# Optimization experiments

Hardware: AMD Instinct MI355X
Metric: run time of the kernel (lower is better)

The kernel has to match this reference:

```python
import jax, jax.numpy as jnp
import numpy as np

EMBED_DIM = 4096
LOW_RANK = 512
BATCH = 8192
K_SEL = 128


def setup_inputs() -> dict:
    key = jax.random.key(0)
    k1, k2, k3, k4 = jax.random.split(key, 4)
    base = jax.random.normal(k1, (BATCH, EMBED_DIM), dtype=jnp.float32)
    source = jax.random.normal(k2, (BATCH, EMBED_DIM), dtype=jnp.float32)
    # fast path: only subspaces[0] is used (all examples share the same index set)
    row = jax.random.randint(k3, (1, K_SEL), 0, LOW_RANK)
    subspaces = jnp.broadcast_to(row, (BATCH, K_SEL)).astype(jnp.int64)
    # orthogonal (column-orthonormal) rotation weight, as produced by
    # torch.nn.utils.parametrizations.orthogonal on [embed_dim, low_rank]
    W, _ = jnp.linalg.qr(jax.random.normal(k4, (EMBED_DIM, LOW_RANK), dtype=jnp.float32))
    return {"base": base, "source": source, "subspaces": subspaces, "W": W}


def reference(base, source, subspaces, W):
    # rotated_base / rotated_source: [B, r]
    # diff in rotated space, gather selected subspace columns, project back.
    sel = subspaces[0]                      # [k] shared index set (fast path)
    diff = (source - base) @ W              # [B, r]
    diff_sel = diff[:, sel]                 # [B, k]
    W_sel = W[:, sel]                       # [d, k]
    out = base + diff_sel @ W_sel.T         # [B, d]
    return out.astype(base.dtype)
```

## Files before the change

### kernel.cpp

```cpp
#include <hip/hip_runtime.h>
#include <hip/hip_bf16.h>

typedef __attribute__((ext_vector_type(4))) float  f32x4;
typedef __attribute__((ext_vector_type(8))) short  short8;
typedef __attribute__((ext_vector_type(4))) short  short4v;

#define EMBED 4096
#define LR    512
#define KSEL  128
#define BATCH 8192

__device__ __forceinline__ short f2bf(float x) {
  union { float f; unsigned u; } c; c.f = x;
  unsigned r = c.u + 0x7FFFu + ((c.u >> 16) & 1u);
  return (short)(r >> 16);
}

__global__ __launch_bounds__(256) void pack_w_kernel(
    const float* __restrict__ W, const int* __restrict__ sel,
    short* __restrict__ Wp, short* __restrict__ Wtp) {
  int idx = blockIdx.x * 256 + threadIdx.x;
  int e = idx >> 7;
  int c = idx & 127;
  int r = sel[c];
  short v = f2bf(W[e * LR + r]);
  Wp [(((e >> 3) << 7) + c) * 8 + (e & 7)] = v;
  Wtp[(((c >> 3) << 12) + e) * 8 + (c & 7)] = v;
}

__global__ __launch_bounds__(256) void gemm1_kernel(
    const float* __restrict__ base, const float* __restrict__ src,
    const short* __restrict__ Wp, short* __restrict__ Tp) {
  __shared__ short Dl[1024];
  const int t  = threadIdx.x;
  const int w  = t >> 6, l = t & 63;
  const int lr = l & 15, lg = l >> 4;
  const int row0 = blockIdx.x * 16;

  const int sr = t >> 4, sk = (t & 15) * 4;
  const float* bp = base + (size_t)(row0 + sr) * EMBED + sk;
  const float* sp = src  + (size_t)(row0 + sr) * EMBED + sk;
  const int wofs = (((sk >> 3) << 4) + sr) * 8 + (sk & 7);

  const short* wpb = Wp + ((lg << 7) + (w << 5) + lr) * 8;

  f32x4 acc0 = {0.f, 0.f, 0.f, 0.f}, acc1 = {0.f, 0.f, 0.f, 0.f};

  f32x4 vb = *(const f32x4*)bp;
  f32x4 vs = *(const f32x4*)sp;

  for (int kt = 0; kt < 64; ++kt) {
    __syncthreads();
    short4v d;
    #pragma unroll
    for (int c = 0; c < 4; ++c) d[c] = f2bf(vs[c] - vb[c]);
    *(short4v*)&Dl[wofs] = d;
    if (kt < 63) {
      vb = *(const f32x4*)(bp + (kt + 1) * 64);
      vs = *(const f32x4*)(sp + (kt + 1) * 64);
    }
    __syncthreads();
    const int kc = kt * 64;
    #pragma unroll
    for (int ks = 0; ks < 2; ++ks) {
      short8 a  = *(const short8*)&Dl[((ks * 4 + lg) << 7) + lr * 8];
      short8 b0 = *(const short8*)(wpb + kc * 128 + ks * 4096);
      short8 b1 = *(const short8*)(wpb + kc * 128 + ks * 4096 + 128);
      acc0 = __builtin_amdgcn_mfma_f32_16x16x32_bf16(a, b0, acc0, 0, 0, 0);
      acc1 = __builtin_amdgcn_mfma_f32_16x16x32_bf16(a, b1, acc1, 0, 0, 0);
    }
  }

  #pragma unroll
  for (int nf = 0; nf < 2; ++nf) {
    f32x4 a = nf ? acc1 : acc0;
    int kk = (w << 5) + (nf << 4) + lr;
    short* dst = Tp + (size_t)(((kk >> 3) << 13) + row0 + (lg << 2)) * 8 + (kk & 7);
    #pragma unroll
    for (int r = 0; r < 4; ++r) dst[r * 8] = f2bf(a[r]);
  }
}

__global__ __launch_bounds__(256) void gemm2_kernel(
    const float* __restrict__ base, const short* __restrict__ Tp,
    const short* __restrict__ Wtp, float* __restrict__ out) {
  const int t  = threadIdx.x;
  const int w  = t >> 6, l = t & 63;
  const int lr = l & 15, lg = l >> 4;
  const int mt = blockIdx.x >> 4, nt = blockIdx.x & 15;
  const int row0 = mt * 64;
  const int col0 = nt * 256 + w * 64;

  short8 afr[4][4];
  #pragma unroll
  for (int m = 0; m < 4; ++m)
    #pragma unroll
    for (int ks = 0; ks < 4; ++ks)
      afr[m][ks] = *(const short8*)(Tp + (size_t)(((ks * 4 + lg) << 13) + row0 + m * 16 + lr) * 8);

  f32x4 acc[4][4];
  #pragma unroll
  for (int m = 0; m < 4; ++m)
    #pragma unroll
    for (int nf = 0; nf < 4; ++nf) acc[m][nf] = (f32x4){0.f, 0.f, 0.f, 0.f};

  #pragma unroll
  for (int nf = 0; nf < 4; ++nf) {
    short8 bfr[4];
    #pragma unroll
    for (int ks = 0; ks < 4; ++ks)
      bfr[ks] = *(const short8*)(Wtp + (size_t)(((ks * 4 + lg) << 12) + col0 + nf * 16 + lr) * 8);
    #pragma unroll
    for (int m = 0; m < 4; ++m)
      #pragma unroll
      for (int ks = 0; ks < 4; ++ks)
        acc[m][nf] = __builtin_amdgcn_mfma_f32_16x16x32_bf16(afr[m][ks], bfr[ks], acc[m][nf], 0, 0, 0);
  }

  #pragma unroll
  for (int m = 0; m < 4; ++m)
    #pragma unroll
    for (int r = 0; r < 4; ++r) {
      const size_t row = row0 + m * 16 + lg * 4 + r;
      #pragma unroll
      for (int nf = 0; nf < 4; ++nf) {
        const size_t o = row * EMBED + col0 + nf * 16 + lr;
        out[o] = base[o] + acc[m][nf][r];
      }
    }
}

extern "C" void kernel_launch(void* const* d_in, const int* in_sizes, int n_in,
                              void* d_out, int out_size, void* d_ws, size_t ws_size,
                              hipStream_t stream) {
  const float* base = (const float*)d_in[0];
  const float* src  = (const float*)d_in[1];
  const int*   sub  = (const int*)d_in[2];
  const float* W    = (const float*)d_in[3];
  float* out = (float*)d_out;

  short* Wp  = (short*)d_ws;
  short* Wtp = Wp  + EMBED * KSEL;
  short* Tp  = Wtp + EMBED * KSEL;

  pack_w_kernel<<<EMBED * KSEL / 256, 256, 0, stream>>>(W, sub, Wp, Wtp);
  gemm1_kernel<<<BATCH / 16, 256, 0, stream>>>(base, src, Wp, Tp);
  gemm2_kernel<<<(BATCH / 64) * 16, 256, 0, stream>>>(base, Tp, Wtp, out);
}
```

Baseline: 140.4 us.

## Split gemm1 K dimension across eight waves with LDS reduction, drop per-step syncs

```diff
diff --git a/kernel.cpp b/kernel.cpp
--- a/kernel.cpp
+++ b/kernel.cpp
@@ -3,7 +3,6 @@
 
 typedef __attribute__((ext_vector_type(4))) float  f32x4;
 typedef __attribute__((ext_vector_type(8))) short  short8;
-typedef __attribute__((ext_vector_type(4))) short  short4v;
 
 #define EMBED 4096
 #define LR    512
@@ -28,56 +27,55 @@
   Wtp[(((c >> 3) << 12) + e) * 8 + (c & 7)] = v;
 }
 
-__global__ __launch_bounds__(256) void gemm1_kernel(
+__global__ __launch_bounds__(512) void gemm1_kernel(
     const float* __restrict__ base, const float* __restrict__ src,
     const short* __restrict__ Wp, short* __restrict__ Tp) {
-  __shared__ short Dl[1024];
+  __shared__ f32x4 red[8 * 8 * 64];
   const int t  = threadIdx.x;
   const int w  = t >> 6, l = t & 63;
   const int lr = l & 15, lg = l >> 4;
   const int row0 = blockIdx.x * 16;
+  const int k0 = w * 512;
 
-  const int sr = t >> 4, sk = (t & 15) * 4;
-  const float* bp = base + (size_t)(row0 + sr) * EMBED + sk;
-  const float* sp = src  + (size_t)(row0 + sr) * EMBED + sk;
-  const int wofs = (((sk >> 3) << 4) + sr) * 8 + (sk & 7);
+  const float* bp = base + (size_t)(row0 + lr) * EMBED + k0 + lg * 8;
+  const float* sp = src  + (size_t)(row0 + lr) * EMBED + k0 + lg * 8;
 
-  const short* wpb = Wp + ((lg << 7) + (w << 5) + lr) * 8;
+  f32x4 acc[8];
+  #pragma unroll
+  for (int nf = 0; nf < 8; ++nf) acc[nf] = (f32x4){0.f, 0.f, 0.f, 0.f};
 
-  f32x4 acc0 = {0.f, 0.f, 0.f, 0.f}, acc1 = {0.f, 0.f, 0.f, 0.f};
-
-  f32x4 vb = *(const f32x4*)bp;
-  f32x4 vs = *(const f32x4*)sp;
-
-  for (int kt = 0; kt < 64; ++kt) {
-    __syncthreads();
-    short4v d;
+  #pragma unroll 4
+  for (int it = 0; it < 16; ++it) {
+    const int kb = it * 32;
+    f32x4 b0 = *(const f32x4*)(bp + kb);
+    f32x4 b1 = *(const f32x4*)(bp + kb + 4);
+    f32x4 s0 = *(const f32x4*)(sp + kb);
+    f32x4 s1 = *(const f32x4*)(sp + kb + 4);
+    short8 a;
     #pragma unroll
-    for (int c = 0; c < 4; ++c) d[c] = f2bf(vs[c] - vb[c]);
-    *(short4v*)&Dl[wofs] = d;
-    if (kt < 63) {
-      vb = *(const f32x4*)(bp + (kt + 1) * 64);
-      vs = *(const f32x4*)(sp + (kt + 1) * 64);
+    for (int j = 0; j < 4; ++j) {
+      a[j]     = f2bf(s0[j] - b0[j]);
+      a[4 + j] = f2bf(s1[j] - b1[j]);
     }
-    __syncthreads();
-    const int kc = kt * 64;
+    const int e = k0 + kb + lg * 8;
+    const short8* wrow = (const short8*)Wp + ((e >> 3) << 7);
     #pragma unroll
-    for (int ks = 0; ks < 2; ++ks) {
-      short8 a  = *(const short8*)&Dl[((ks * 4 + lg) << 7) + lr * 8];
-      short8 b0 = *(const short8*)(wpb + kc * 128 + ks * 4096);
-      short8 b1 = *(const short8*)(wpb + kc * 128 + ks * 4096 + 128);
-      acc0 = __builtin_amdgcn_mfma_f32_16x16x32_bf16(a, b0, acc0, 0, 0, 0);
-      acc1 = __builtin_amdgcn_mfma_f32_16x16x32_bf16(a, b1, acc1, 0, 0, 0);
-    }
+    for (int nf = 0; nf < 8; ++nf)
+      acc[nf] = __builtin_amdgcn_mfma_f32_16x16x32_bf16(a, wrow[nf * 16 + lr], acc[nf], 0, 0, 0);
   }
 
   #pragma unroll
-  for (int nf = 0; nf < 2; ++nf) {
-    f32x4 a = nf ? acc1 : acc0;
-    int kk = (w << 5) + (nf << 4) + lr;
-    short* dst = Tp + (size_t)(((kk >> 3) << 13) + row0 + (lg << 2)) * 8 + (kk & 7);
+  for (int nf = 0; nf < 8; ++nf) red[(w << 9) + (nf << 6) + l] = acc[nf];
+  __syncthreads();
+  {
+    const int rl = t & 63, rnf = t >> 6;
+    f32x4 s = red[(rnf << 6) + rl];
     #pragma unroll
-    for (int r = 0; r < 4; ++r) dst[r * 8] = f2bf(a[r]);
+    for (int w2 = 1; w2 < 8; ++w2) s += red[(w2 << 9) + (rnf << 6) + rl];
+    const int kk = rnf * 16 + (rl & 15);
+    short* dst = Tp + (size_t)(((kk >> 3) << 13) + row0 + ((rl >> 4) << 2)) * 8 + (kk & 7);
+    #pragma unroll
+    for (int r = 0; r < 4; ++r) dst[r * 8] = f2bf(s[r]);
   }
 }
 
@@ -144,6 +142,6 @@
   short* Tp  = Wtp + EMBED * KSEL;
 
   pack_w_kernel<<<EMBED * KSEL / 256, 256, 0, stream>>>(W, sub, Wp, Wtp);
-  gemm1_kernel<<<BATCH / 16, 256, 0, stream>>>(base, src, Wp, Tp);
+  gemm1_kernel<<<BATCH / 16, 512, 0, stream>>>(base, src, Wp, Tp);
   gemm2_kernel<<<(BATCH / 64) * 16, 256, 0, stream>>>(base, Tp, Wtp, out);
 }
```

Result: no change. 140.2 us (-0.1%).

## Split first GEMM over K slices with register-held weights and a reduction pass

Applied to the files above, without the earlier changes.

```diff
diff --git a/kernel.cpp b/kernel.cpp
--- a/kernel.cpp
+++ b/kernel.cpp
@@ -9,11 +9,27 @@
 #define LR    512
 #define KSEL  128
 #define BATCH 8192
+#define NSLICE 8
+#define KSLICE 512
 
 __device__ __forceinline__ short f2bf(float x) {
   union { float f; unsigned u; } c; c.f = x;
   unsigned r = c.u + 0x7FFFu + ((c.u >> 16) & 1u);
   return (short)(r >> 16);
+}
+__device__ __forceinline__ float bf2f(short s) {
+  union { unsigned u; float f; } c; c.u = ((unsigned)(unsigned short)s) << 16;
+  return c.f;
+}
+__device__ __forceinline__ void storept(float* p, float v) { *p = v; }
+__device__ __forceinline__ void storept(short* p, float v) { *p = f2bf(v); }
+__device__ __forceinline__ void loadpart(const float* p, f32x4& a, f32x4& b) {
+  a += *(const f32x4*)p; b += *(const f32x4*)(p + 4);
+}
+__device__ __forceinline__ void loadpart(const short* p, f32x4& a, f32x4& b) {
+  short8 v = *(const short8*)p;
+  #pragma unroll
+  for (int j = 0; j < 4; ++j) { a[j] += bf2f(v[j]); b[j] += bf2f(v[4 + j]); }
 }
 
 __global__ __launch_bounds__(256) void pack_w_kernel(
@@ -28,57 +44,86 @@
   Wtp[(((c >> 3) << 12) + e) * 8 + (c & 7)] = v;
 }
 
-__global__ __launch_bounds__(256) void gemm1_kernel(
+template<typename PT>
+__global__ __launch_bounds__(512, 4) void gemm1a_kernel(
     const float* __restrict__ base, const float* __restrict__ src,
-    const short* __restrict__ Wp, short* __restrict__ Tp) {
-  __shared__ short Dl[1024];
+    const short* __restrict__ Wp, PT* __restrict__ Tpart) {
+  __shared__ __align__(16) short D[2 * 2048];
   const int t  = threadIdx.x;
   const int w  = t >> 6, l = t & 63;
   const int lr = l & 15, lg = l >> 4;
-  const int row0 = blockIdx.x * 16;
-
-  const int sr = t >> 4, sk = (t & 15) * 4;
-  const float* bp = base + (size_t)(row0 + sr) * EMBED + sk;
-  const float* sp = src  + (size_t)(row0 + sr) * EMBED + sk;
-  const int wofs = (((sk >> 3) << 4) + sr) * 8 + (sk & 7);
-
-  const short* wpb = Wp + ((lg << 7) + (w << 5) + lr) * 8;
-
-  f32x4 acc0 = {0.f, 0.f, 0.f, 0.f}, acc1 = {0.f, 0.f, 0.f, 0.f};
-
-  f32x4 vb = *(const f32x4*)bp;
-  f32x4 vs = *(const f32x4*)sp;
-
-  for (int kt = 0; kt < 64; ++kt) {
-    __syncthreads();
-    short4v d;
-    #pragma unroll
-    for (int c = 0; c < 4; ++c) d[c] = f2bf(vs[c] - vb[c]);
-    *(short4v*)&Dl[wofs] = d;
-    if (kt < 63) {
-      vb = *(const f32x4*)(bp + (kt + 1) * 64);
-      vs = *(const f32x4*)(sp + (kt + 1) * 64);
-    }
-    __syncthreads();
-    const int kc = kt * 64;
-    #pragma unroll
-    for (int ks = 0; ks < 2; ++ks) {
-      short8 a  = *(const short8*)&Dl[((ks * 4 + lg) << 7) + lr * 8];
-      short8 b0 = *(const short8*)(wpb + kc * 128 + ks * 4096);
-      short8 b1 = *(const short8*)(wpb + kc * 128 + ks * 4096 + 128);
-      acc0 = __builtin_amdgcn_mfma_f32_16x16x32_bf16(a, b0, acc0, 0, 0, 0);
-      acc1 = __builtin_amdgcn_mfma_f32_16x16x32_bf16(a, b1, acc1, 0, 0, 0);
-    }
+  const int rg = blockIdx.x & 63, slice = blockIdx.x >> 6;
+  const int row0 = rg * 128;
+  const int k0 = slice * KSLICE;
+
+  short8 bfr[16];
+  #pragma unroll
+  for (int kg = 0; kg < 16; ++kg)
+    bfr[kg] = *(const short8*)(Wp + (((((k0 >> 3) + kg * 4 + lg)) << 7) + w * 16 + lr) * 8);
+
+  const int srow  = t >> 5;
+  const int sbyte = srow * 256 + ((((t & 31) >> 1) ^ (srow & 7)) << 4) + (t & 1) * 8;
+  const float* bp = base + (size_t)(row0 + srow) * EMBED + k0 + (t & 31) * 4;
+  const float* sp = src  + (size_t)(row0 + srow) * EMBED + k0 + (t & 31) * 4;
+
+  const int rsw = (lr & 7) << 4;
+  const char* tb = (const char*)D + lr * 256;
+
+  f32x4 vbA = *(const f32x4*)bp,          vsA = *(const f32x4*)sp;
+  f32x4 vbB = *(const f32x4*)(bp + 128),  vsB = *(const f32x4*)(sp + 128);
+
+  f32x4 acc = {0.f, 0.f, 0.f, 0.f};
+  PT* tout = Tpart + (size_t)slice * BATCH * KSEL + (size_t)(row0 + lg * 4) * KSEL + w * 16 + lr;
+
+  #define KSTEP(BUF, VB, VS, KG0, PF_OK, PF_OFF)                              \
+    do {                                                                      \
+      short4v d;                                                              \
+      _Pragma("unroll")                                                       \
+      for (int j = 0; j < 4; ++j) d[j] = f2bf(VS[j] - VB[j]);                 \
+      *(short4v*)((char*)D + (BUF) * 4096 + sbyte) = d;                       \
+      if (PF_OK) {                                                            \
+        VB = *(const f32x4*)(bt + (PF_OFF));                                  \
+        VS = *(const f32x4*)(st + (PF_OFF));                                  \
+      }                                                                       \
+      __syncthreads();                                                        \
+      _Pragma("unroll")                                                       \
+      for (int kg = 0; kg < 4; ++kg) {                                        \
+        short8 a = *(const short8*)(tb + (BUF) * 4096 +                       \
+                                    ((kg * 64 + lg * 16) ^ rsw));             \
+        acc = __builtin_amdgcn_mfma_f32_16x16x32_bf16(a, bfr[(KG0) + kg],     \
+                                                      acc, 0, 0, 0);          \
+      }                                                                       \
+    } while (0)
+
+  for (int tile = 0; tile < 8; ++tile) {
+    const float* bt = bp + (size_t)tile * 16 * EMBED;
+    const float* st = sp + (size_t)tile * 16 * EMBED;
+    const bool pf = (tile < 7);
+    KSTEP(0, vbA, vsA, 0,  true, 256);
+    KSTEP(1, vbB, vsB, 4,  true, 384);
+    KSTEP(0, vbA, vsA, 8,  pf,   16 * EMBED);
+    KSTEP(1, vbB, vsB, 12, pf,   16 * EMBED + 128);
+    PT* o = tout + (size_t)tile * 16 * KSEL;
+    #pragma unroll
+    for (int r = 0; r < 4; ++r) storept(o + (size_t)r * KSEL, acc[r]);
+    acc = (f32x4){0.f, 0.f, 0.f, 0.f};
   }
-
-  #pragma unroll
-  for (int nf = 0; nf < 2; ++nf) {
-    f32x4 a = nf ? acc1 : acc0;
-    int kk = (w << 5) + (nf << 4) + lr;
-    short* dst = Tp + (size_t)(((kk >> 3) << 13) + row0 + (lg << 2)) * 8 + (kk & 7);
-    #pragma unroll
-    for (int r = 0; r < 4; ++r) dst[r * 8] = f2bf(a[r]);
-  }
+  #undef KSTEP
+}
+
+template<typename PT>
+__global__ __launch_bounds__(512) void reduce_kernel(
+    const PT* __restrict__ Tpart, short* __restrict__ Tp) {
+  const int tid = blockIdx.x * 512 + threadIdx.x;
+  const int kkg = tid & 15, row = tid >> 4;
+  f32x4 s0 = {0.f, 0.f, 0.f, 0.f}, s1 = {0.f, 0.f, 0.f, 0.f};
+  #pragma unroll
+  for (int s = 0; s < NSLICE; ++s)
+    loadpart(Tpart + ((size_t)s * BATCH + row) * KSEL + kkg * 8, s0, s1);
+  short8 o;
+  #pragma unroll
+  for (int j = 0; j < 4; ++j) { o[j] = f2bf(s0[j]); o[4 + j] = f2bf(s1[j]); }
+  *(short8*)(Tp + ((size_t)kkg * BATCH + row) * 8) = o;
 }
 
 __global__ __launch_bounds__(256) void gemm2_kernel(
@@ -142,8 +187,21 @@
   short* Wp  = (short*)d_ws;
   short* Wtp = Wp  + EMBED * KSEL;
   short* Tp  = Wtp + EMBED * KSEL;
+  char*  rest = (char*)(Tp + BATCH * KSEL);
 
   pack_w_kernel<<<EMBED * KSEL / 256, 256, 0, stream>>>(W, sub, Wp, Wtp);
-  gemm1_kernel<<<BATCH / 16, 256, 0, stream>>>(base, src, Wp, Tp);
+
+  const size_t need_f32 = (size_t)4 * 1024 * 1024 +
+                          (size_t)NSLICE * BATCH * KSEL * sizeof(float);
+  if (ws_size >= need_f32) {
+    float* Tpart = (float*)rest;
+    gemm1a_kernel<float><<<512, 512, 0, stream>>>(base, src, Wp, Tpart);
+    reduce_kernel<float><<<BATCH * 16 / 512, 512, 0, stream>>>(Tpart, Tp);
+  } else {
+    short* Tpart = (short*)rest;
+    gemm1a_kernel<short><<<512, 512, 0, stream>>>(base, src, Wp, Tpart);
+    reduce_kernel<short><<<BATCH * 16 / 512, 512, 0, stream>>>(Tpart, Tp);
+  }
+
   gemm2_kernel<<<(BATCH / 64) * 16, 256, 0, stream>>>(base, Tp, Wtp, out);
 }
```

After: 126.0 us. 10.2% less time.

## Stage gemm1 inputs into LDS with async double-buffered global loads

Applied to the files above, without the earlier changes.

```diff
diff --git a/kernel.cpp b/kernel.cpp
--- a/kernel.cpp
+++ b/kernel.cpp
@@ -3,7 +3,7 @@
 
 typedef __attribute__((ext_vector_type(4))) float  f32x4;
 typedef __attribute__((ext_vector_type(8))) short  short8;
-typedef __attribute__((ext_vector_type(4))) short  short4v;
+typedef unsigned int u32;
 
 #define EMBED 4096
 #define LR    512
@@ -14,6 +14,10 @@
   union { float f; unsigned u; } c; c.f = x;
   unsigned r = c.u + 0x7FFFu + ((c.u >> 16) & 1u);
   return (short)(r >> 16);
+}
+__device__ __forceinline__ void gload16(const void* g, void* l) {
+  __builtin_amdgcn_global_load_lds((const __attribute__((address_space(1))) u32*)g,
+                                   (__attribute__((address_space(3))) u32*)l, 16, 0, 0);
 }
 
 __global__ __launch_bounds__(256) void pack_w_kernel(
@@ -28,53 +32,71 @@
   Wtp[(((c >> 3) << 12) + e) * 8 + (c & 7)] = v;
 }
 
-__global__ __launch_bounds__(256) void gemm1_kernel(
+__global__ __launch_bounds__(256, 2) void gemm1_kernel(
     const float* __restrict__ base, const float* __restrict__ src,
     const short* __restrict__ Wp, short* __restrict__ Tp) {
-  __shared__ short Dl[1024];
+  __shared__ __align__(16) char smem[65536];
   const int t  = threadIdx.x;
   const int w  = t >> 6, l = t & 63;
   const int lr = l & 15, lg = l >> 4;
   const int row0 = blockIdx.x * 16;
 
-  const int sr = t >> 4, sk = (t & 15) * 4;
-  const float* bp = base + (size_t)(row0 + sr) * EMBED + sk;
-  const float* sp = src  + (size_t)(row0 + sr) * EMBED + sk;
-  const int wofs = (((sk >> 3) << 4) + sr) * 8 + (sk & 7);
+  const int srow = t >> 6;
+  const int sc   = t & 63;
 
-  const short* wpb = Wp + ((lg << 7) + (w << 5) + lr) * 8;
+  #define STAGE(s, b) do {                                                  \
+    char* d_ = smem + (b) * 32768 + t * 16;                                 \
+    _Pragma("unroll")                                                       \
+    for (int i = 0; i < 4; ++i) {                                           \
+      const int row = i * 4 + srow;                                         \
+      const size_t go = (size_t)(row0 + row) * EMBED + (s) * 256            \
+                        + ((sc ^ (row & 7)) << 2);                          \
+      gload16(base + go, d_ + i * 4096);                                    \
+      gload16(src  + go, d_ + 16384 + i * 4096);                            \
+    }                                                                       \
+  } while (0)
 
+  const short8* wq = (const short8*)Wp;
   f32x4 acc0 = {0.f, 0.f, 0.f, 0.f}, acc1 = {0.f, 0.f, 0.f, 0.f};
 
-  f32x4 vb = *(const f32x4*)bp;
-  f32x4 vs = *(const f32x4*)sp;
-
-  for (int kt = 0; kt < 64; ++kt) {
+  STAGE(0, 0);
+  int b = 0;
+  for (int s = 0; s < 16; ++s) {
     __syncthreads();
-    short4v d;
+    const int kc = s * 256;
+    short8 bf[16];
     #pragma unroll
-    for (int c = 0; c < 4; ++c) d[c] = f2bf(vs[c] - vb[c]);
-    *(short4v*)&Dl[wofs] = d;
-    if (kt < 63) {
-      vb = *(const f32x4*)(bp + (kt + 1) * 64);
-      vs = *(const f32x4*)(sp + (kt + 1) * 64);
+    for (int kstep = 0; kstep < 8; ++kstep) {
+      const int kg = ((kc + kstep * 32) >> 3) + lg;
+      bf[kstep * 2]     = wq[(size_t)kg * 128 + w * 32 + lr];
+      bf[kstep * 2 + 1] = wq[(size_t)kg * 128 + w * 32 + 16 + lr];
     }
-    __syncthreads();
-    const int kc = kt * 64;
+    if (s < 15) STAGE(s + 1, b ^ 1);
+    const char* tb = smem + b * 32768 + lr * 1024;
     #pragma unroll
-    for (int ks = 0; ks < 2; ++ks) {
-      short8 a  = *(const short8*)&Dl[((ks * 4 + lg) << 7) + lr * 8];
-      short8 b0 = *(const short8*)(wpb + kc * 128 + ks * 4096);
-      short8 b1 = *(const short8*)(wpb + kc * 128 + ks * 4096 + 128);
-      acc0 = __builtin_amdgcn_mfma_f32_16x16x32_bf16(a, b0, acc0, 0, 0, 0);
-      acc1 = __builtin_amdgcn_mfma_f32_16x16x32_bf16(a, b1, acc1, 0, 0, 0);
+    for (int kstep = 0; kstep < 8; ++kstep) {
+      const int j0 = (kstep * 8 + lg * 2)     ^ (lr & 7);
+      const int j1 = (kstep * 8 + lg * 2 + 1) ^ (lr & 7);
+      f32x4 b0 = *(const f32x4*)(tb + j0 * 16);
+      f32x4 b1 = *(const f32x4*)(tb + j1 * 16);
+      f32x4 s0 = *(const f32x4*)(tb + 16384 + j0 * 16);
+      f32x4 s1 = *(const f32x4*)(tb + 16384 + j1 * 16);
+      union { short8 v; __hip_bfloat162 h[4]; } u;
+      u.h[0] = __float22bfloat162_rn(make_float2(s0[0] - b0[0], s0[1] - b0[1]));
+      u.h[1] = __float22bfloat162_rn(make_float2(s0[2] - b0[2], s0[3] - b0[3]));
+      u.h[2] = __float22bfloat162_rn(make_float2(s1[0] - b1[0], s1[1] - b1[1]));
+      u.h[3] = __float22bfloat162_rn(make_float2(s1[2] - b1[2], s1[3] - b1[3]));
+      acc0 = __builtin_amdgcn_mfma_f32_16x16x32_bf16(u.v, bf[kstep * 2],     acc0, 0, 0, 0);
+      acc1 = __builtin_amdgcn_mfma_f32_16x16x32_bf16(u.v, bf[kstep * 2 + 1], acc1, 0, 0, 0);
     }
+    b ^= 1;
   }
+  #undef STAGE
 
   #pragma unroll
-  for (int nf = 0; nf < 2; ++nf) {
-    f32x4 a = nf ? acc1 : acc0;
-    int kk = (w << 5) + (nf << 4) + lr;
+  for (int ct = 0; ct < 2; ++ct) {
+    f32x4 a = ct ? acc1 : acc0;
+    const int kk = w * 32 + ct * 16 + lr;
     short* dst = Tp + (size_t)(((kk >> 3) << 13) + row0 + (lg << 2)) * 8 + (kk & 7);
     #pragma unroll
     for (int r = 0; r < 4; ++r) dst[r * 8] = f2bf(a[r]);
```

After: 135.0 us. 3.8% less time.
